# Performance work log

Hardware: AMD Instinct MI355X
Metric: run time of the kernel (lower is better)

The kernel has to match this reference:

```python
import jax, jax.numpy as jnp
jax.config.update("jax_enable_x64", True)
import numpy as np

B = 1_000_000

def _basis_and_weights():
    # 7 Lie-algebra generators of the homography group (4x4), as in the torch module
    E = np.zeros((7, 4, 4), dtype=np.float64)
    E[0, 0, 3] = 1.0   # x translation
    E[1, 1, 3] = 1.0   # y translation
    E[2, 2, 3] = 1.0   # z translation
    E[3, 1, 2] = -1.0; E[3, 2, 1] = 1.0   # yz rotation generator
    E[4, 0, 2] = 1.0;  E[4, 2, 0] = -1.0  # xz rotation generator
    E[5, 0, 1] = -1.0; E[5, 1, 0] = 1.0   # xy rotation generator
    E[6, 0, 0] = 1.0;  E[6, 1, 1] = -1.0  # xy stretch generator
    w = np.ones((7,), dtype=np.float64)   # all *_weight init kwargs = 1.0
    return jnp.asarray(E), jnp.asarray(w)


def setup_inputs() -> dict:
    key = jax.random.key(0)
    lie_vectors = jax.random.normal(key, (B, 7), dtype=jnp.float32)
    return {"lie_vectors": lie_vectors}


def reference(lie_vectors):
    elements, weights = _basis_and_weights()
    # weighted sum of basis elements: (B,7) x (7,4,4) -> (B,4,4), in float64 (dtype_cast_to)
    A = jnp.einsum("bk,kij->bij", lie_vectors.astype(jnp.float64) * weights, elements)
    # batched 4x4 matrix exponential
    T = jax.vmap(jax.scipy.linalg.expm)(A)
    # homogeneous normalization by the (3,3) entry
    T = T / T[:, 3:4, 3:4]
    return T.astype(jnp.float32)  # dtype_out
```

## Files before the change

### kernel.cpp

```cpp
#include <hip/hip_runtime.h>
#include <math.h>

#define BLOCK 256

__global__ __launch_bounds__(BLOCK) void lie_expm_kernel(
    const float* __restrict__ in, float* __restrict__ out, int B)
{
    __shared__ float sh[BLOCK * 7];
    const int tid = threadIdx.x;
    const long long blockBase = (long long)blockIdx.x * BLOCK;

    {
        const long long gbase = blockBase * 7;
        int valid = B - (int)blockBase;
        if (valid > BLOCK) valid = BLOCK;
        const int limit = valid * 7;
        for (int i = tid; i < BLOCK * 7; i += BLOCK)
            sh[i] = (i < limit) ? in[gbase + i] : 0.0f;
    }
    __syncthreads();

    const int b = (int)blockBase + tid;
    if (b >= B) return;

    const double v0 = (double)sh[tid * 7 + 0];
    const double v1 = (double)sh[tid * 7 + 1];
    const double v2 = (double)sh[tid * 7 + 2];
    const double v3 = (double)sh[tid * 7 + 3];
    const double v4 = (double)sh[tid * 7 + 4];
    const double v5 = (double)sh[tid * 7 + 5];
    const double v6 = (double)sh[tid * 7 + 6];

    double X[3][4] = {
        {  v6, -v5,  v4, v0 },
        {  v5, -v6, -v3, v1 },
        { -v4,  v3, 0.0, v2 }
    };

    double n0 = fabs(X[0][0]) + fabs(X[0][1]) + fabs(X[0][2]) + fabs(X[0][3]);
    double n1 = fabs(X[1][0]) + fabs(X[1][1]) + fabs(X[1][2]) + fabs(X[1][3]);
    double n2 = fabs(X[2][0]) + fabs(X[2][1]) + fabs(X[2][2]) + fabs(X[2][3]);
    double nrm = fmax(n0, fmax(n1, n2));

    int s = 0;
    if (nrm > 0.5) s = ilogb(nrm) + 2;
    const double sc = ldexp(1.0, -s);
    #pragma unroll
    for (int i = 0; i < 3; i++)
        #pragma unroll
        for (int c = 0; c < 4; c++)
            X[i][c] *= sc;

    double P[3][4] = { {1,0,0,0}, {0,1,0,0}, {0,0,1,0} };
    #pragma unroll
    for (int k = 13; k >= 1; k--) {
        double T[3][4];
        #pragma unroll
        for (int i = 0; i < 3; i++) {
            #pragma unroll
            for (int c = 0; c < 4; c++) {
                double acc = (c == 3) ? X[i][3] : 0.0;
                acc = fma(X[i][0], P[0][c], acc);
                acc = fma(X[i][1], P[1][c], acc);
                acc = fma(X[i][2], P[2][c], acc);
                T[i][c] = acc;
            }
        }
        const double invk = 1.0 / (double)k;
        #pragma unroll
        for (int i = 0; i < 3; i++)
            #pragma unroll
            for (int c = 0; c < 4; c++)
                P[i][c] = ((i == c) ? 1.0 : 0.0) + T[i][c] * invk;
    }

    for (int q = 0; q < s; q++) {
        double T[3][4];
        #pragma unroll
        for (int i = 0; i < 3; i++) {
            #pragma unroll
            for (int c = 0; c < 4; c++) {
                double acc = (c == 3) ? P[i][3] : 0.0;
                acc = fma(P[i][0], P[0][c], acc);
                acc = fma(P[i][1], P[1][c], acc);
                acc = fma(P[i][2], P[2][c], acc);
                T[i][c] = acc;
            }
        }
        #pragma unroll
        for (int i = 0; i < 3; i++)
            #pragma unroll
            for (int c = 0; c < 4; c++)
                P[i][c] = T[i][c];
    }

    float4* o = (float4*)(out + (long long)b * 16);
    o[0] = make_float4((float)P[0][0], (float)P[0][1], (float)P[0][2], (float)P[0][3]);
    o[1] = make_float4((float)P[1][0], (float)P[1][1], (float)P[1][2], (float)P[1][3]);
    o[2] = make_float4((float)P[2][0], (float)P[2][1], (float)P[2][2], (float)P[2][3]);
    o[3] = make_float4(0.0f, 0.0f, 0.0f, 1.0f);
}

extern "C" void kernel_launch(void* const* d_in, const int* in_sizes, int n_in,
                              void* d_out, int out_size, void* d_ws, size_t ws_size,
                              hipStream_t stream) {
    const float* in = (const float*)d_in[0];
    float* out = (float*)d_out;
    const int B = in_sizes[0] / 7;
    const int grid = (B + BLOCK - 1) / BLOCK;
    lie_expm_kernel<<<grid, BLOCK, 0, stream>>>(in, out, B);
}
```

Measured before the change: 108.9 us.

## Compute Lie matrix exponential in fp32 with shorter Taylor series

Switches all per-element arithmetic (scaling, Taylor series, squaring) from double to float and reduces the Taylor expansion from 13 to 9 terms. This targets the fp64 ALU cost that dominates this compute-bound kernel. It risks larger numerical error versus the float64 reference, especially after repeated squaring for large-norm inputs.

```diff
diff --git a/kernel.cpp b/kernel.cpp
--- a/kernel.cpp
+++ b/kernel.cpp
@@ -23,67 +23,67 @@
     const int b = (int)blockBase + tid;
     if (b >= B) return;
 
-    const double v0 = (double)sh[tid * 7 + 0];
-    const double v1 = (double)sh[tid * 7 + 1];
-    const double v2 = (double)sh[tid * 7 + 2];
-    const double v3 = (double)sh[tid * 7 + 3];
-    const double v4 = (double)sh[tid * 7 + 4];
-    const double v5 = (double)sh[tid * 7 + 5];
-    const double v6 = (double)sh[tid * 7 + 6];
+    const float v0 = sh[tid * 7 + 0];
+    const float v1 = sh[tid * 7 + 1];
+    const float v2 = sh[tid * 7 + 2];
+    const float v3 = sh[tid * 7 + 3];
+    const float v4 = sh[tid * 7 + 4];
+    const float v5 = sh[tid * 7 + 5];
+    const float v6 = sh[tid * 7 + 6];
 
-    double X[3][4] = {
+    float X[3][4] = {
         {  v6, -v5,  v4, v0 },
         {  v5, -v6, -v3, v1 },
-        { -v4,  v3, 0.0, v2 }
+        { -v4,  v3, 0.0f, v2 }
     };
 
-    double n0 = fabs(X[0][0]) + fabs(X[0][1]) + fabs(X[0][2]) + fabs(X[0][3]);
-    double n1 = fabs(X[1][0]) + fabs(X[1][1]) + fabs(X[1][2]) + fabs(X[1][3]);
-    double n2 = fabs(X[2][0]) + fabs(X[2][1]) + fabs(X[2][2]) + fabs(X[2][3]);
-    double nrm = fmax(n0, fmax(n1, n2));
+    float n0 = fabsf(X[0][0]) + fabsf(X[0][1]) + fabsf(X[0][2]) + fabsf(X[0][3]);
+    float n1 = fabsf(X[1][0]) + fabsf(X[1][1]) + fabsf(X[1][2]) + fabsf(X[1][3]);
+    float n2 = fabsf(X[2][0]) + fabsf(X[2][1]) + fabsf(X[2][2]) + fabsf(X[2][3]);
+    float nrm = fmaxf(n0, fmaxf(n1, n2));
 
     int s = 0;
-    if (nrm > 0.5) s = ilogb(nrm) + 2;
-    const double sc = ldexp(1.0, -s);
+    if (nrm > 0.5f) s = ilogbf(nrm) + 2;
+    const float sc = ldexpf(1.0f, -s);
     #pragma unroll
     for (int i = 0; i < 3; i++)
         #pragma unroll
         for (int c = 0; c < 4; c++)
             X[i][c] *= sc;
 
-    double P[3][4] = { {1,0,0,0}, {0,1,0,0}, {0,0,1,0} };
+    float P[3][4] = { {1,0,0,0}, {0,1,0,0}, {0,0,1,0} };
     #pragma unroll
-    for (int k = 13; k >= 1; k--) {
-        double T[3][4];
+    for (int k = 9; k >= 1; k--) {
+        float T[3][4];
         #pragma unroll
         for (int i = 0; i < 3; i++) {
             #pragma unroll
             for (int c = 0; c < 4; c++) {
-                double acc = (c == 3) ? X[i][3] : 0.0;
-                acc = fma(X[i][0], P[0][c], acc);
-                acc = fma(X[i][1], P[1][c], acc);
-                acc = fma(X[i][2], P[2][c], acc);
+                float acc = (c == 3) ? X[i][3] : 0.0f;
+                acc = fmaf(X[i][0], P[0][c], acc);
+                acc = fmaf(X[i][1], P[1][c], acc);
+                acc = fmaf(X[i][2], P[2][c], acc);
                 T[i][c] = acc;
             }
         }
-        const double invk = 1.0 / (double)k;
+        const float invk = 1.0f / (float)k;
         #pragma unroll
         for (int i = 0; i < 3; i++)
             #pragma unroll
             for (int c = 0; c < 4; c++)
-                P[i][c] = ((i == c) ? 1.0 : 0.0) + T[i][c] * invk;
+                P[i][c] = ((i == c) ? 1.0f : 0.0f) + T[i][c] * invk;
     }
 
     for (int q = 0; q < s; q++) {
-        double T[3][4];
+        float T[3][4];
         #pragma unroll
         for (int i = 0; i < 3; i++) {
             #pragma unroll
             for (int c = 0; c < 4; c++) {
-                double acc = (c == 3) ? P[i][3] : 0.0;
-                acc = fma(P[i][0], P[0][c], acc);
-                acc = fma(P[i][1], P[1][c], acc);
-                acc = fma(P[i][2], P[2][c], acc);
+                float acc = (c == 3) ? P[i][3] : 0.0f;
+                acc = fmaf(P[i][0], P[0][c], acc);
+                acc = fmaf(P[i][1], P[1][c], acc);
+                acc = fmaf(P[i][2], P[2][c], acc);
                 T[i][c] = acc;
             }
         }
@@ -95,9 +95,9 @@
     }
 
     float4* o = (float4*)(out + (long long)b * 16);
-    o[0] = make_float4((float)P[0][0], (float)P[0][1], (float)P[0][2], (float)P[0][3]);
-    o[1] = make_float4((float)P[1][0], (float)P[1][1], (float)P[1][2], (float)P[1][3]);
-    o[2] = make_float4((float)P[2][0], (float)P[2][1], (float)P[2][2], (float)P[2][3]);
+    o[0] = make_float4(P[0][0], P[0][1], P[0][2], P[0][3]);
+    o[1] = make_float4(P[1][0], P[1][1], P[1][2], P[1][3]);
+    o[2] = make_float4(P[2][0], P[2][1], P[2][2], P[2][3]);
     o[3] = make_float4(0.0f, 0.0f, 0.0f, 1.0f);
 }
 
```

Result: faster. 101.4 us (-6.9%).
